# Kernel optimization log

Measured on AMD Instinct MI355X. Metric: run time of the kernel, lower is better.

Reference implementation:

```python
import jax, jax.numpy as jnp
import numpy as np

B, N, O, K, F = 4, 256, 5, 5, 256
H, D, DFF = 4, 64, 1024  # num_heads, KQ_len, FFN hidden
EPS = 1e-5


def setup_inputs() -> dict:
    key = jax.random.key(0)
    ks = jax.random.split(key, 16)
    s = 0.05
    p = lambda k, shape: (jax.random.normal(k, shape, jnp.float32) * s)
    return {
        "x": jax.random.normal(ks[0], (B, N, O, K, K, F), jnp.float32),
        "Wq": p(ks[1], (H * D, F)), "bq": p(ks[2], (H * D,)),
        "Wk": p(ks[3], (H * D, F)), "bk": p(ks[4], (H * D,)),
        "Wv": p(ks[5], (H * D, F)), "bv": p(ks[6], (H * D,)),
        "Wf": p(ks[7], (F, F)), "bf": p(ks[8], (F,)),
        "ln1_w": jnp.ones((N, O, F), jnp.float32), "ln1_b": jnp.zeros((N, O, F), jnp.float32),
        "ln2_w": jnp.ones((N, O, F), jnp.float32), "ln2_b": jnp.zeros((N, O, F), jnp.float32),
        "W1": p(ks[9], (DFF, F)), "b1": p(ks[10], (DFF,)),
        "W2": p(ks[11], (F, DFF)), "b2": p(ks[12], (F,)),
    }


def _layer_norm3(x, w, b):
    # torch LayerNorm with normalized_shape=[N, O, F]: stats over last 3 dims
    mu = jnp.mean(x, axis=(1, 2, 3), keepdims=True)
    var = jnp.var(x, axis=(1, 2, 3), keepdims=True)
    return (x - mu) * jax.lax.rsqrt(var + EPS) * w + b


def _split_heads(y):
    # [B,N,O,K,K,H*D] -> [B,N,O,H,K,K,D]
    return y.reshape(B, N, O, K, K, H, D).transpose(0, 1, 2, 5, 3, 4, 6)


def reference(x, Wq, bq, Wk, bk, Wv, bv, Wf, bf,
              ln1_w, ln1_b, ln2_w, ln2_b, W1, b1, W2, b2):
    q = _split_heads(x @ Wq.T + bq)
    k = _split_heads(x @ Wk.T + bk)
    v = _split_heads(x @ Wv.T + bv)
    c = K // 2
    qc = q[:, :, :, :, c, c, :]  # center query [B,N,O,H,D]
    # tile+mul+sum == dot of center query against every patch key
    scores = jnp.einsum('bnohd,bnohijd->bnohij', qc, k) / np.sqrt(float(D))
    w = jax.nn.softmax(scores.reshape(B, N, O, H, K * K), axis=-1)
    merged = jnp.einsum('bnohp,bnohpd->bnohd', w, v.reshape(B, N, O, H, K * K, D))
    merged = merged.reshape(B, N, O, H * D)
    attent = merged @ Wf.T + bf  # dropout = identity (eval)
    out1 = _layer_norm3(attent, ln1_w, ln1_b)
    ffn = jax.nn.relu(out1 @ W1.T + b1) @ W2.T + b2
    return _layer_norm3(out1 + ffn, ln2_w, ln2_b)
```

## Files before the change

### kernel.cpp

```cpp
#include <hip/hip_runtime.h>
#include <hip/hip_bf16.h>

#define FF 256
#define HH 4
#define DD 64
#define PP 25
#define SITES 5120
#define SPB 1280
#define DFF 1024
#define LN_ELEMS 327680

typedef const __hip_bfloat16* bfp;
typedef __hip_bfloat16* bfw;
typedef __attribute__((ext_vector_type(8))) short bf16x8;
typedef __attribute__((ext_vector_type(4))) float f32x4;

__device__ __forceinline__ float b2f(const __hip_bfloat16 v) { return __bfloat162float(v); }
__device__ __forceinline__ bool detect_bf(const unsigned* dt) {
    return dt[0] == 0x3F803F80u;
}
__device__ __forceinline__ float ldin(const void* p, size_t i, bool bf) {
    return bf ? __bfloat162float(((const __hip_bfloat16*)p)[i]) : ((const float*)p)[i];
}
__device__ __forceinline__ unsigned short f2bu(float f) {
    __hip_bfloat16 h = __float2bfloat16(f);
    return *(unsigned short*)&h;
}
__device__ __forceinline__ uint4 ldin8(const void* p, size_t i, bool bf) {
    if (bf) return *(const uint4*)((const unsigned short*)p + i);
    const float* f = (const float*)p + i;
    const float4 a = *(const float4*)f;
    const float4 b = *(const float4*)(f + 4);
    unsigned short u[8] = { f2bu(a.x), f2bu(a.y), f2bu(a.z), f2bu(a.w),
                            f2bu(b.x), f2bu(b.y), f2bu(b.z), f2bu(b.w) };
    return *(uint4*)u;
}
__device__ __forceinline__ void ldin8v(const void* p, size_t i, bool bf, float* o) {
    if (bf) {
        const uint4 v = *(const uint4*)((const unsigned short*)p + i);
        const unsigned short* u = (const unsigned short*)&v;
        #pragma unroll
        for (int j = 0; j < 8; ++j) o[j] = __bfloat162float(*(const __hip_bfloat16*)&u[j]);
    } else {
        const float4 a = *(const float4*)((const float*)p + i);
        const float4 b = *(const float4*)((const float*)p + i + 4);
        o[0]=a.x; o[1]=a.y; o[2]=a.z; o[3]=a.w; o[4]=b.x; o[5]=b.y; o[6]=b.z; o[7]=b.w;
    }
}

__global__ __launch_bounds__(256) void prep_k(
    const void* Wq, const void* bq, const void* Wk,
    const void* Wv, const void* bv, const void* Wf, const void* bfv,
    bfw Qeff, float* qb, bfw Weff, float* beff, const unsigned* dt)
{
    const bool bf = detect_bf(dt);
    const int b = blockIdx.x;
    const int t = threadIdx.x;
    if (b < 1024) {
        const int h = b >> 8, f = b & 255;
        __shared__ float wkcol[DD];
        if (t < DD) wkcol[t] = ldin(Wk, (size_t)(h * DD + t) * FF + f, bf);
        __syncthreads();
        float acc = 0.f;
        #pragma unroll 8
        for (int d = 0; d < DD; ++d)
            acc = fmaf(wkcol[d], ldin(Wq, (size_t)(h * DD + d) * FF + t, bf), acc);
        Qeff[(size_t)b * FF + t] = __float2bfloat16(acc);
        if (t == 0) {
            float a = 0.f;
            #pragma unroll 8
            for (int d = 0; d < DD; ++d) a = fmaf(ldin(bq, h * DD + d, bf), wkcol[d], a);
            qb[b] = a;
        }
    } else {
        const int j = b - 1024;
        __shared__ float wfrow[FF];
        wfrow[t] = ldin(Wf, (size_t)j * FF + t, bf);
        __syncthreads();
        #pragma unroll
        for (int h = 0; h < HH; ++h) {
            float acc = 0.f;
            #pragma unroll 8
            for (int d = 0; d < DD; ++d)
                acc = fmaf(wfrow[h * DD + d], ldin(Wv, (size_t)(h * DD + d) * FF + t, bf), acc);
            Weff[(size_t)j * DFF + h * FF + t] = __float2bfloat16(acc);
        }
        if (t == 0) {
            float a = ldin(bfv, j, bf);
            #pragma unroll 8
            for (int i = 0; i < FF; ++i) a = fmaf(wfrow[i], ldin(bv, i, bf), a);
            beff[j] = a;
        }
    }
}

template<int RELU, int RESMODE, int GATHER, int STATS, int BINT, int BIASF, int LNA>
__global__ __launch_bounds__(256) void gemm_mfma(
    const void* Ag, int lda,
    const void* Bm, int ldb, const void* bias,
    const void* resid, int ldr,
    bfw C, int ldc, int Kc,
    const float* lnred, const void* lnw, const void* lnb,
    float* red_out, const unsigned* dt)
{
    const bool bf = detect_bf(dt);
    __shared__ unsigned short Als[64][72];
    __shared__ unsigned short Bls[64][72];
    __shared__ float rs4[4], rss4[4];
    const int tid = threadIdx.x;
    const int lane = tid & 63;
    const int w = tid >> 6;
    const int m0 = blockIdx.y * 64;
    const int n0 = blockIdx.x * 64;
    const int r8 = tid >> 3;
    const int c8 = (tid & 7) * 8;

    const int batch_ = m0 / SPB;
    float mu_ = 0.f, rsc_ = 0.f;
    if (LNA || RESMODE == 2) {
        const float inv = 1.f / (float)LN_ELEMS;
        mu_ = lnred[batch_ * 2] * inv;
        const float var = lnred[batch_ * 2 + 1] * inv - mu_ * mu_;
        rsc_ = rsqrtf(var + 1e-5f);
    }

    f32x4 acc[4];
    #pragma unroll
    for (int mi = 0; mi < 4; ++mi) acc[mi] = (f32x4){0.f, 0.f, 0.f, 0.f};

    for (int k0 = 0; k0 < Kc; k0 += 64) {
        #pragma unroll
        for (int rr = 0; rr < 2; ++rr) {
            const int row = r8 + rr * 32;
            const int grow = m0 + row;
            uint4 v;
            if (GATHER) {
                v = ldin8(Ag, ((size_t)grow * PP + 12) * FF + (k0 + c8), bf);
            } else if (LNA) {
                const int r_ = grow - batch_ * SPB;
                const uint4 av = *(const uint4*)((const unsigned short*)Ag + (size_t)grow * lda + k0 + c8);
                const unsigned short* au = (const unsigned short*)&av;
                float wv8[8], bv8[8];
                ldin8v(lnw, (size_t)r_ * FF + k0 + c8, bf, wv8);
                ldin8v(lnb, (size_t)r_ * FF + k0 + c8, bf, bv8);
                unsigned short o[8];
                #pragma unroll
                for (int j = 0; j < 8; ++j) {
                    const float xf = __bfloat162float(*(const __hip_bfloat16*)&au[j]);
                    o[j] = f2bu((xf - mu_) * rsc_ * wv8[j] + bv8[j]);
                }
                v = *(uint4*)o;
            } else {
                v = *(const uint4*)((const unsigned short*)Ag + (size_t)grow * lda + k0 + c8);
            }
            *(uint4*)&Als[row][c8] = v;
        }
        #pragma unroll
        for (int rr = 0; rr < 2; ++rr) {
            const int row = r8 + rr * 32;
            const size_t bi = (size_t)(n0 + row) * ldb + (k0 + c8);
            uint4 v;
            if (BINT) v = *(const uint4*)((const unsigned short*)Bm + bi);
            else      v = ldin8(Bm, bi, bf);
            *(uint4*)&Bls[row][c8] = v;
        }
        __syncthreads();
        #pragma unroll
        for (int ks = 0; ks < 2; ++ks) {
            const int kq = ks * 32 + (lane >> 4) * 8;
            const bf16x8 bfr = *(const bf16x8*)&Bls[w * 16 + (lane & 15)][kq];
            #pragma unroll
            for (int mi = 0; mi < 4; ++mi) {
                const bf16x8 afr = *(const bf16x8*)&Als[mi * 16 + (lane & 15)][kq];
                acc[mi] = __builtin_amdgcn_mfma_f32_16x16x32_bf16(afr, bfr, acc[mi], 0, 0, 0);
            }
        }
        __syncthreads();
    }

    const int col = n0 + w * 16 + (lane & 15);
    const int quad = lane >> 4;
    float bvv = 0.f;
    if (bias) bvv = BIASF ? ((const float*)bias)[col] : ldin(bias, col, bf);
    float s_ = 0.f, ss_ = 0.f;
    #pragma unroll
    for (int mi = 0; mi < 4; ++mi) {
        #pragma unroll
        for (int r = 0; r < 4; ++r) {
            const int row = m0 + mi * 16 + quad * 4 + r;
            float v = acc[mi][r] + bvv;
            if (RESMODE == 2) {
                const int r_ = row - batch_ * SPB;
                const float af = b2f(((bfp)resid)[(size_t)row * ldr + col]);
                v += (af - mu_) * rsc_ * ldin(lnw, (size_t)r_ * FF + col, bf)
                     + ldin(lnb, (size_t)r_ * FF + col, bf);
            }
            if (RELU) v = fmaxf(v, 0.0f);
            if (STATS) { s_ += v; ss_ += v * v; }
            C[(size_t)row * ldc + col] = __float2bfloat16(v);
        }
    }
    if (STATS) {
        #pragma unroll
        for (int o = 32; o > 0; o >>= 1) { s_ += __shfl_down(s_, o); ss_ += __shfl_down(ss_, o); }
        if (lane == 0) { rs4[w] = s_; rss4[w] = ss_; }
        __syncthreads();
        if (tid == 0) {
            atomicAdd(&red_out[batch_ * 2 + 0], rs4[0] + rs4[1] + rs4[2] + rs4[3]);
            atomicAdd(&red_out[batch_ * 2 + 1], rss4[0] + rss4[1] + rss4[2] + rss4[3]);
        }
    }
}

__global__ __launch_bounds__(256) void attn_site(const void* x, bfp qk, bfw xw,
                                                 const unsigned* dt)
{
    __shared__ unsigned short xsb[32][264];
    __shared__ unsigned short qkb[HH][FF];
    __shared__ float sc[HH][32];
    __shared__ float wl[HH][PP];

    const bool bf = detect_bf(dt);
    const int s = blockIdx.x;
    const int t = threadIdx.x;

    const size_t xbase = (size_t)s * (PP * FF);
    for (int e0 = t * 8; e0 < PP * FF; e0 += 2048)
        *(uint4*)&xsb[e0 >> 8][e0 & 255] = ldin8(x, xbase + e0, bf);
    if (t < 128)
        ((uint4*)qkb)[t] = ((const uint4*)(qk + (size_t)s * (HH * FF)))[t];
    __syncthreads();

    if (t < 64) {
        const int col = t & 15;
        const int quad = t >> 4;
        const int brow = col & 3;
        f32x4 a0v = (f32x4){0.f, 0.f, 0.f, 0.f};
        f32x4 a1v = (f32x4){0.f, 0.f, 0.f, 0.f};
        #pragma unroll
        for (int ks = 0; ks < 8; ++ks) {
            const int kq = ks * 32 + quad * 8;
            const bf16x8 bfr = *(const bf16x8*)&qkb[brow][kq];
            const bf16x8 af0 = *(const bf16x8*)&xsb[col][kq];
            const bf16x8 af1 = *(const bf16x8*)&xsb[16 + col][kq];
            a0v = __builtin_amdgcn_mfma_f32_16x16x32_bf16(af0, bfr, a0v, 0, 0, 0);
            a1v = __builtin_amdgcn_mfma_f32_16x16x32_bf16(af1, bfr, a1v, 0, 0, 0);
        }
        if (col < HH) {
            #pragma unroll
            for (int r = 0; r < 4; ++r) {
                const int p = quad * 4 + r;
                sc[col][p] = a0v[r] * 0.125f;
                const int p2 = 16 + p;
                if (p2 < PP) sc[col][p2] = a1v[r] * 0.125f;
            }
        }
    }
    __syncthreads();

    if (t < HH) {
        float m = -1e30f;
        #pragma unroll
        for (int p = 0; p < PP; ++p) m = fmaxf(m, sc[t][p]);
        float e[PP], ssum = 0.f;
        #pragma unroll
        for (int p = 0; p < PP; ++p) { e[p] = __expf(sc[t][p] - m); ssum += e[p]; }
        const float inv = 1.f / ssum;
        #pragma unroll
        for (int p = 0; p < PP; ++p) wl[t][p] = e[p] * inv;
    }
    __syncthreads();

    float a0 = 0.f, a1 = 0.f, a2 = 0.f, a3 = 0.f;
    #pragma unroll
    for (int p = 0; p < PP; ++p) {
        const float xv = __bfloat162float(*(const __hip_bfloat16*)&xsb[p][t]);
        a0 = fmaf(wl[0][p], xv, a0);
        a1 = fmaf(wl[1][p], xv, a1);
        a2 = fmaf(wl[2][p], xv, a2);
        a3 = fmaf(wl[3][p], xv, a3);
    }
    bfw xwp = xw + (size_t)s * (HH * FF) + t;
    xwp[0 * FF] = __float2bfloat16(a0);
    xwp[1 * FF] = __float2bfloat16(a1);
    xwp[2 * FF] = __float2bfloat16(a2);
    xwp[3 * FF] = __float2bfloat16(a3);
}

__global__ __launch_bounds__(256) void ln_final(bfp X, const float* __restrict__ red,
                                                const void* w, const void* b,
                                                void* out, const unsigned* dt)
{
    const bool bf = detect_bf(dt);
    const int i8 = (blockIdx.x * 256 + threadIdx.x) * 8;
    const int s = i8 >> 8;
    const int batch = s / SPB;
    const int r = s - batch * SPB;
    const int f = i8 & 255;
    const float inv = 1.f / (float)LN_ELEMS;
    const float mu = red[batch * 2] * inv;
    const float var = red[batch * 2 + 1] * inv - mu * mu;
    const float rs = rsqrtf(var + 1e-5f);

    const uint4 xv = *(const uint4*)(X + i8);
    const unsigned short* xu = (const unsigned short*)&xv;
    float wv[8], bv[8], vo[8];
    ldin8v(w, (size_t)r * FF + f, bf, wv);
    ldin8v(b, (size_t)r * FF + f, bf, bv);
    #pragma unroll
    for (int j = 0; j < 8; ++j) {
        const float xf = __bfloat162float(*(const __hip_bfloat16*)&xu[j]);
        vo[j] = (xf - mu) * rs * wv[j] + bv[j];
    }
    if (!bf) {
        float* o = (float*)out + i8;
        *(float4*)o = (float4){vo[0], vo[1], vo[2], vo[3]};
        *(float4*)(o + 4) = (float4){vo[4], vo[5], vo[6], vo[7]};
    } else {
        unsigned short ou[8];
        #pragma unroll
        for (int j = 0; j < 8; ++j) ou[j] = f2bu(vo[j]);
        *(uint4*)((unsigned short*)out + i8) = *(uint4*)ou;
    }
}

extern "C" void kernel_launch(void* const* d_in, const int* in_sizes, int n_in,
                              void* d_out, int out_size, void* d_ws, size_t ws_size,
                              hipStream_t stream)
{
    const void* x    = d_in[0];
    const void* Wq   = d_in[1];
    const void* bq   = d_in[2];
    const void* Wk   = d_in[3];
    const void* Wv   = d_in[5];
    const void* bv   = d_in[6];
    const void* Wf   = d_in[7];
    const void* bfv  = d_in[8];
    const void* ln1w = d_in[9];
    const void* ln1b = d_in[10];
    const void* ln2w = d_in[11];
    const void* ln2b = d_in[12];
    const void* W1   = d_in[13];
    const void* b1   = d_in[14];
    const void* W2   = d_in[15];
    const void* b2   = d_in[16];
    const unsigned* dt = (const unsigned*)d_in[9];

    char* w8 = (char*)d_ws;
    bfw qk   = (bfw)(w8);
    bfw xw   = (bfw)(w8 + 10485760);
    bfw hid  = (bfw)(w8 + 20971520);
    bfw att  = (bfw)(w8 + 31457280);
    bfw z    = (bfw)(w8 + 34078720);
    bfw Qeff = (bfw)(w8 + 36700160);
    bfw Weff = (bfw)(w8 + 37224448);
    float* qb   = (float*)(w8 + 37748736);
    float* beff = (float*)(w8 + 37752832);
    float* red  = (float*)(w8 + 37753856);

    hipMemsetAsync(red, 0, 64, stream);

    prep_k<<<1280, 256, 0, stream>>>(Wq, bq, Wk, Wv, bv, Wf, bfv,
                                     Qeff, qb, Weff, beff, dt);

    gemm_mfma<0, 0, 1, 0, 1, 1, 0><<<dim3(16, 80), 256, 0, stream>>>(
        x, 0, Qeff, FF, qb, nullptr, 0, qk, DFF, FF,
        nullptr, nullptr, nullptr, nullptr, dt);

    attn_site<<<SITES, 256, 0, stream>>>(x, qk, xw, dt);

    gemm_mfma<0, 0, 0, 1, 1, 1, 0><<<dim3(4, 80), 256, 0, stream>>>(
        xw, DFF, Weff, DFF, beff, nullptr, 0, att, FF, DFF,
        nullptr, nullptr, nullptr, red, dt);

    gemm_mfma<1, 0, 0, 0, 0, 0, 1><<<dim3(16, 80), 256, 0, stream>>>(
        att, FF, W1, FF, b1, nullptr, 0, hid, DFF, FF,
        red, ln1w, ln1b, nullptr, dt);

    gemm_mfma<0, 2, 0, 1, 0, 0, 0><<<dim3(4, 80), 256, 0, stream>>>(
        hid, DFF, W2, DFF, b2, att, FF, z, FF, DFF,
        red, ln1w, ln1b, red + 8, dt);

    ln_final<<<640, 256, 0, stream>>>(z, red + 8, ln2w, ln2b, d_out, dt);
}
```

Before: 379.8 us.

## Widen GEMM K-tile to 256, pre-gather center rows, fold memset into prep

The GEMM K-step grows from 64 to 256, so each block loads a 64x256 tile of A and B per iteration and crosses four times fewer barriers. This raises LDS use to about 67KB per block, and launch bounds are set to target two blocks per CU. The center-pixel gather of x moves into extra prep_k blocks that write a compact bf16 copy, so the first GEMM reads contiguous rows. The reduction buffer is now zeroed inside prep_k instead of by a separate memset, which removes one stream operation.

```diff
diff --git a/kernel.cpp b/kernel.cpp
--- a/kernel.cpp
+++ b/kernel.cpp
@@ -49,13 +49,15 @@
 }
 
 __global__ __launch_bounds__(256) void prep_k(
-    const void* Wq, const void* bq, const void* Wk,
+    const void* x, const void* Wq, const void* bq, const void* Wk,
     const void* Wv, const void* bv, const void* Wf, const void* bfv,
-    bfw Qeff, float* qb, bfw Weff, float* beff, const unsigned* dt)
+    bfw Qeff, float* qb, bfw Weff, float* beff, bfw xc, float* red,
+    const unsigned* dt)
 {
     const bool bf = detect_bf(dt);
     const int b = blockIdx.x;
     const int t = threadIdx.x;
+    if (b == 0 && t < 16) red[t] = 0.f;
     if (b < 1024) {
         const int h = b >> 8, f = b & 255;
         __shared__ float wkcol[DD];
@@ -72,7 +74,7 @@
             for (int d = 0; d < DD; ++d) a = fmaf(ldin(bq, h * DD + d, bf), wkcol[d], a);
             qb[b] = a;
         }
-    } else {
+    } else if (b < 1280) {
         const int j = b - 1024;
         __shared__ float wfrow[FF];
         wfrow[t] = ldin(Wf, (size_t)j * FF + t, bf);
@@ -91,12 +93,21 @@
             for (int i = 0; i < FF; ++i) a = fmaf(wfrow[i], ldin(bv, i, bf), a);
             beff[j] = a;
         }
-    }
-}
-
-template<int RELU, int RESMODE, int GATHER, int STATS, int BINT, int BIASF, int LNA>
-__global__ __launch_bounds__(256) void gemm_mfma(
-    const void* Ag, int lda,
+    } else {
+        const int s0 = (b - 1280) * 64;
+        #pragma unroll
+        for (int it = 0; it < 8; ++it) {
+            const int e0 = t * 8 + it * 2048;
+            const int srow = e0 >> 8, col = e0 & 255;
+            *(uint4*)(xc + (size_t)(s0 + srow) * FF + col) =
+                ldin8(x, ((size_t)(s0 + srow) * PP + 12) * FF + col, bf);
+        }
+    }
+}
+
+template<int RELU, int RESMODE, int STATS, int BINT, int BIASF, int LNA>
+__global__ __launch_bounds__(256, 2) void gemm_mfma(
+    bfp Ag, int lda,
     const void* Bm, int ldb, const void* bias,
     const void* resid, int ldr,
     bfw C, int ldc, int Kc,
@@ -104,16 +115,15 @@
     float* red_out, const unsigned* dt)
 {
     const bool bf = detect_bf(dt);
-    __shared__ unsigned short Als[64][72];
-    __shared__ unsigned short Bls[64][72];
+    __shared__ unsigned short Als[64][264];
+    __shared__ unsigned short Bls[64][264];
     __shared__ float rs4[4], rss4[4];
     const int tid = threadIdx.x;
     const int lane = tid & 63;
     const int w = tid >> 6;
+    const int quad = lane >> 4;
     const int m0 = blockIdx.y * 64;
     const int n0 = blockIdx.x * 64;
-    const int r8 = tid >> 3;
-    const int c8 = (tid & 7) * 8;
 
     const int batch_ = m0 / SPB;
     float mu_ = 0.f, rsc_ = 0.f;
@@ -128,21 +138,20 @@
     #pragma unroll
     for (int mi = 0; mi < 4; ++mi) acc[mi] = (f32x4){0.f, 0.f, 0.f, 0.f};
 
-    for (int k0 = 0; k0 < Kc; k0 += 64) {
-        #pragma unroll
-        for (int rr = 0; rr < 2; ++rr) {
-            const int row = r8 + rr * 32;
+    for (int k0 = 0; k0 < Kc; k0 += 256) {
+        if (k0) __syncthreads();
+        #pragma unroll
+        for (int it = 0; it < 8; ++it) {
+            const int e0 = tid * 8 + it * 2048;
+            const int row = e0 >> 8, col = e0 & 255;
             const int grow = m0 + row;
-            uint4 v;
-            if (GATHER) {
-                v = ldin8(Ag, ((size_t)grow * PP + 12) * FF + (k0 + c8), bf);
-            } else if (LNA) {
+            uint4 v = *(const uint4*)((const unsigned short*)Ag + (size_t)grow * lda + k0 + col);
+            if (LNA) {
                 const int r_ = grow - batch_ * SPB;
-                const uint4 av = *(const uint4*)((const unsigned short*)Ag + (size_t)grow * lda + k0 + c8);
-                const unsigned short* au = (const unsigned short*)&av;
+                const unsigned short* au = (const unsigned short*)&v;
                 float wv8[8], bv8[8];
-                ldin8v(lnw, (size_t)r_ * FF + k0 + c8, bf, wv8);
-                ldin8v(lnb, (size_t)r_ * FF + k0 + c8, bf, bv8);
+                ldin8v(lnw, (size_t)r_ * FF + col, bf, wv8);
+                ldin8v(lnb, (size_t)r_ * FF + col, bf, bv8);
                 unsigned short o[8];
                 #pragma unroll
                 for (int j = 0; j < 8; ++j) {
@@ -150,24 +159,23 @@
                     o[j] = f2bu((xf - mu_) * rsc_ * wv8[j] + bv8[j]);
                 }
                 v = *(uint4*)o;
-            } else {
-                v = *(const uint4*)((const unsigned short*)Ag + (size_t)grow * lda + k0 + c8);
             }
-            *(uint4*)&Als[row][c8] = v;
-        }
-        #pragma unroll
-        for (int rr = 0; rr < 2; ++rr) {
-            const int row = r8 + rr * 32;
-            const size_t bi = (size_t)(n0 + row) * ldb + (k0 + c8);
+            *(uint4*)&Als[row][col] = v;
+        }
+        #pragma unroll
+        for (int it = 0; it < 8; ++it) {
+            const int e0 = tid * 8 + it * 2048;
+            const int row = e0 >> 8, col = e0 & 255;
+            const size_t bi = (size_t)(n0 + row) * ldb + k0 + col;
             uint4 v;
             if (BINT) v = *(const uint4*)((const unsigned short*)Bm + bi);
             else      v = ldin8(Bm, bi, bf);
-            *(uint4*)&Bls[row][c8] = v;
+            *(uint4*)&Bls[row][col] = v;
         }
         __syncthreads();
         #pragma unroll
-        for (int ks = 0; ks < 2; ++ks) {
-            const int kq = ks * 32 + (lane >> 4) * 8;
+        for (int kc = 0; kc < 8; ++kc) {
+            const int kq = kc * 32 + quad * 8;
             const bf16x8 bfr = *(const bf16x8*)&Bls[w * 16 + (lane & 15)][kq];
             #pragma unroll
             for (int mi = 0; mi < 4; ++mi) {
@@ -175,11 +183,9 @@
                 acc[mi] = __builtin_amdgcn_mfma_f32_16x16x32_bf16(afr, bfr, acc[mi], 0, 0, 0);
             }
         }
-        __syncthreads();
     }
 
     const int col = n0 + w * 16 + (lane & 15);
-    const int quad = lane >> 4;
     float bvv = 0.f;
     if (bias) bvv = BIASF ? ((const float*)bias)[col] : ldin(bias, col, bf);
     float s_ = 0.f, ss_ = 0.f;
@@ -354,30 +360,29 @@
     bfw z    = (bfw)(w8 + 34078720);
     bfw Qeff = (bfw)(w8 + 36700160);
     bfw Weff = (bfw)(w8 + 37224448);
-    float* qb   = (float*)(w8 + 37748736);
-    float* beff = (float*)(w8 + 37752832);
-    float* red  = (float*)(w8 + 37753856);
-
-    hipMemsetAsync(red, 0, 64, stream);
-
-    prep_k<<<1280, 256, 0, stream>>>(Wq, bq, Wk, Wv, bv, Wf, bfv,
-                                     Qeff, qb, Weff, beff, dt);
-
-    gemm_mfma<0, 0, 1, 0, 1, 1, 0><<<dim3(16, 80), 256, 0, stream>>>(
-        x, 0, Qeff, FF, qb, nullptr, 0, qk, DFF, FF,
+    bfw xc   = (bfw)(w8 + 37748736);
+    float* qb   = (float*)(w8 + 40370176);
+    float* beff = (float*)(w8 + 40374272);
+    float* red  = (float*)(w8 + 40375296);
+
+    prep_k<<<1360, 256, 0, stream>>>(x, Wq, bq, Wk, Wv, bv, Wf, bfv,
+                                     Qeff, qb, Weff, beff, xc, red, dt);
+
+    gemm_mfma<0, 0, 0, 1, 1, 0><<<dim3(16, 80), 256, 0, stream>>>(
+        xc, FF, Qeff, FF, qb, nullptr, 0, qk, DFF, FF,
         nullptr, nullptr, nullptr, nullptr, dt);
 
     attn_site<<<SITES, 256, 0, stream>>>(x, qk, xw, dt);
 
-    gemm_mfma<0, 0, 0, 1, 1, 1, 0><<<dim3(4, 80), 256, 0, stream>>>(
+    gemm_mfma<0, 0, 1, 1, 1, 0><<<dim3(4, 80), 256, 0, stream>>>(
         xw, DFF, Weff, DFF, beff, nullptr, 0, att, FF, DFF,
         nullptr, nullptr, nullptr, red, dt);
 
-    gemm_mfma<1, 0, 0, 0, 0, 0, 1><<<dim3(16, 80), 256, 0, stream>>>(
+    gemm_mfma<1, 0, 0, 0, 0, 1><<<dim3(16, 80), 256, 0, stream>>>(
         att, FF, W1, FF, b1, nullptr, 0, hid, DFF, FF,
         red, ln1w, ln1b, nullptr, dt);
 
-    gemm_mfma<0, 2, 0, 1, 0, 0, 0><<<dim3(4, 80), 256, 0, stream>>>(
+    gemm_mfma<0, 2, 1, 0, 0, 0><<<dim3(4, 80), 256, 0, stream>>>(
         hid, DFF, W2, DFF, b2, att, FF, z, FF, DFF,
         red, ln1w, ln1b, red + 8, dt);
 
```

Measured after the change: 363.0 us. 4.4% less time.
